# Optimization experiments

Measured on AMD Instinct MI355X. Metric: run time of the kernel, lower is better.

Reference implementation:

```python
import jax, jax.numpy as jnp
import numpy as np

B, N, T = 64, 256, 512          # batch, num_objs, num_triples
DO, DP, H, DOUT = 512, 512, 512, 512


def setup_inputs() -> dict:
    key = jax.random.key(0)
    ks = jax.random.split(key, 12)

    def kaiming(k, shape):
        fan_in = shape[0]
        return jax.random.normal(k, shape, jnp.float32) * np.sqrt(2.0 / fan_in)

    return {
        "obj_vecs": jax.random.normal(ks[0], (B, N, DO), jnp.float32),
        "pred_vecs": jax.random.normal(ks[1], (B, T, DP), jnp.float32),
        "edges": jax.random.randint(ks[2], (B, T, 3), 0, N, jnp.int64),
        # net1: [2*DO+DP -> H -> 2*H+DOUT], ReLU after each Linear
        "n1_w1": kaiming(ks[3], (2 * DO + DP, H)),
        "n1_b1": jnp.zeros((H,), jnp.float32),
        "n1_w2": kaiming(ks[4], (H, 2 * H + DOUT)),
        "n1_b2": jnp.zeros((2 * H + DOUT,), jnp.float32),
        # net2: [H -> H -> DOUT], ReLU after each Linear
        "n2_w1": kaiming(ks[5], (H, H)),
        "n2_b1": jnp.zeros((H,), jnp.float32),
        "n2_w2": kaiming(ks[6], (H, DOUT)),
        "n2_b2": jnp.zeros((DOUT,), jnp.float32),
    }


def reference(obj_vecs, pred_vecs, edges,
              n1_w1, n1_b1, n1_w2, n1_b2,
              n2_w1, n2_b1, n2_w2, n2_b2):
    num_batch, num_objs, _ = obj_vecs.shape
    h_dim = n1_b1.shape[0]
    d_out = n2_w2.shape[1]

    s_idx = edges[:, :, 0]            # [B, T] subject node ids
    o_idx = edges[:, :, 2]            # [B, T] object node ids

    # gather subject/object vectors per triple
    cur_s = jnp.take_along_axis(obj_vecs, s_idx[:, :, None], axis=1)  # [B,T,DO]
    cur_o = jnp.take_along_axis(obj_vecs, o_idx[:, :, None], axis=1)  # [B,T,DO]
    cur_t = jnp.concatenate([cur_s, pred_vecs, cur_o], axis=-1)       # [B,T,2DO+DP]

    # net1 MLP (Linear+ReLU, Linear+ReLU)
    hid = jax.nn.relu(jnp.einsum('btd,dh->bth', cur_t, n1_w1) + n1_b1)
    new_t = jax.nn.relu(jnp.einsum('bth,hk->btk', hid, n1_w2) + n1_b2)

    new_s = new_t[:, :, :h_dim]
    new_p = new_t[:, :, h_dim:h_dim + d_out]
    new_o = new_t[:, :, h_dim + d_out:2 * h_dim + d_out]

    # scatter-add back to nodes, per batch element
    b_ix = jnp.arange(num_batch)[:, None]            # [B,1]
    pooled = jnp.zeros((num_batch, num_objs, h_dim), obj_vecs.dtype)
    pooled = pooled.at[b_ix, s_idx].add(new_s)
    pooled = pooled.at[b_ix, o_idx].add(new_o)

    # avg pooling: divide by per-node incidence count (clamped at 1)
    ones = jnp.ones(s_idx.shape, obj_vecs.dtype)
    counts = jnp.zeros((num_batch, num_objs), obj_vecs.dtype)
    counts = counts.at[b_ix, s_idx].add(ones)
    counts = counts.at[b_ix, o_idx].add(ones)
    counts = jnp.maximum(counts, 1.0)
    pooled = pooled / counts[:, :, None]

    # net2 MLP (Linear+ReLU, Linear+ReLU)
    h2 = jax.nn.relu(jnp.einsum('bnh,hk->bnk', pooled, n2_w1) + n2_b1)
    new_obj_vecs = jax.nn.relu(jnp.einsum('bnh,hd->bnd', h2, n2_w2) + n2_b2)

    return new_obj_vecs, new_p
```

## Files before the change

### kernel.cpp

```cpp
#include <hip/hip_runtime.h>

typedef __bf16 bf16;
typedef __attribute__((ext_vector_type(4))) __bf16 bf16x4;
typedef __attribute__((ext_vector_type(8))) __bf16 bf16x8;
typedef __attribute__((ext_vector_type(4))) float f32x4;

#define DEVINL __device__ __forceinline__

typedef __attribute__((address_space(1))) void gvoid_t;
typedef __attribute__((address_space(3))) void lvoid_t;

DEVINL void async_ld16(const void* g, void* l) {
    __builtin_amdgcn_global_load_lds((gvoid_t*)g, (lvoid_t*)l, 16, 0, 0);
}

template<int MODE, int NBN>
__global__ __launch_bounds__(256, 2) void gemm_k(
    const bf16* __restrict__ A, const bf16* __restrict__ Bt,
    const float* __restrict__ bias, bf16* __restrict__ Dbf,
    float* __restrict__ Df, bf16* __restrict__ Dbf2,
    const int* __restrict__ edges, const bf16* __restrict__ obj,
    const bf16* __restrict__ pred, int K)
{
    const int tid = threadIdx.x;
    const int id = blockIdx.x;
    const int bn = (id >> 3) % NBN;
    const int bm = (id & 7) + 8 * ((id >> 3) / NBN);

    __shared__ __align__(16) bf16 ldsA[128 * 64];
    __shared__ __align__(16) bf16 ldsB[128 * 64];

    const int g_slot = tid & 7;
    const int row0 = tid >> 3;

    unsigned offS[4], offP[4], offO[4], offA[4], offB[4];
#pragma unroll
    for (int i = 0; i < 4; i++) {
        int r = row0 + 32 * i;
        int gr = bm * 128 + r;
        if (MODE == 0) {
            int b = gr >> 9;
            int s = edges[gr * 3 + 0] & 255;
            int o = edges[gr * 3 + 2] & 255;
            offS[i] = (unsigned)(b * 256 + s) * 512u;
            offP[i] = (unsigned)gr * 512u;
            offO[i] = (unsigned)(b * 256 + o) * 512u;
        } else {
            offA[i] = (unsigned)gr * (unsigned)K;
        }
        offB[i] = (unsigned)(bn * 128 + r) * (unsigned)K;
    }

    f32x4 acc[4][4];
    const f32x4 zero4 = {0.f, 0.f, 0.f, 0.f};
#pragma unroll
    for (int i = 0; i < 4; i++)
#pragma unroll
        for (int j = 0; j < 4; j++) acc[i][j] = zero4;

    const int wave = tid >> 6;
    const int lane = tid & 63;
    const int wr = (wave >> 1) * 64;
    const int wc = (wave & 1) * 64;
    const int lq = lane >> 4;
    const int lr = lane & 15;

    const int KT = K >> 6;
    for (int kt = 0; kt < KT; ++kt) {
        __syncthreads();
#pragma unroll
        for (int i = 0; i < 4; i++) {
            int r = row0 + 32 * i;
            int gsrc = g_slot ^ (r & 7);
            const bf16* gp;
            if (MODE == 0) {
                int region = kt >> 3;
                unsigned col = (unsigned)((kt & 7) * 64 + gsrc * 8);
                if (region == 0)      gp = obj + offS[i] + col;
                else if (region == 1) gp = pred + offP[i] + col;
                else                  gp = obj + offO[i] + col;
            } else {
                gp = A + offA[i] + (unsigned)(kt * 64 + gsrc * 8);
            }
            async_ld16(gp, ldsA + (tid + i * 256) * 8);
        }
#pragma unroll
        for (int i = 0; i < 4; i++) {
            int r = row0 + 32 * i;
            int gsrc = g_slot ^ (r & 7);
            async_ld16(Bt + offB[i] + (unsigned)(kt * 64 + gsrc * 8),
                       ldsB + (tid + i * 256) * 8);
        }
        __syncthreads();

#pragma unroll
        for (int ks = 0; ks < 2; ++ks) {
            bf16x8 af[4], bfr[4];
#pragma unroll
            for (int mi = 0; mi < 4; ++mi) {
                int r = wr + mi * 16 + lr;
                int g = (ks * 4 + lq) ^ (r & 7);
                af[mi] = *(const bf16x8*)(ldsA + (r * 8 + g) * 8);
            }
#pragma unroll
            for (int ni = 0; ni < 4; ++ni) {
                int r = wc + ni * 16 + lr;
                int g = (ks * 4 + lq) ^ (r & 7);
                bfr[ni] = *(const bf16x8*)(ldsB + (r * 8 + g) * 8);
            }
#pragma unroll
            for (int mi = 0; mi < 4; ++mi)
#pragma unroll
                for (int ni = 0; ni < 4; ++ni)
                    acc[mi][ni] = __builtin_amdgcn_mfma_f32_16x16x32_bf16(
                        bfr[ni], af[mi], acc[mi][ni], 0, 0, 0);
        }
    }

#pragma unroll
    for (int ni = 0; ni < 4; ++ni) {
        int col = bn * 128 + wc + ni * 16 + lq * 4;
        const f32x4 bv = *(const f32x4*)(bias + col);
#pragma unroll
        for (int mi = 0; mi < 4; ++mi) {
            int row = bm * 128 + wr + mi * 16 + lr;
            f32x4 v = acc[mi][ni];
            f32x4 x;
#pragma unroll
            for (int r = 0; r < 4; r++) {
                float t = v[r] + bv[r];
                x[r] = t > 0.f ? t : 0.f;
            }
            if (MODE == 1) {
                if (col < 512) {
                    bf16x4 o = { (bf16)x[0], (bf16)x[1], (bf16)x[2], (bf16)x[3] };
                    *(bf16x4*)(Dbf + row * 512 + col) = o;
                } else if (col < 1024) {
                    *(f32x4*)(Df + row * 512 + (col - 512)) = x;
                } else {
                    bf16x4 o = { (bf16)x[0], (bf16)x[1], (bf16)x[2], (bf16)x[3] };
                    *(bf16x4*)(Dbf2 + row * 512 + (col - 1024)) = o;
                }
            } else if (MODE == 3) {
                *(f32x4*)(Df + row * 512 + col) = x;
            } else {
                bf16x4 o = { (bf16)x[0], (bf16)x[1], (bf16)x[2], (bf16)x[3] };
                *(bf16x4*)(Dbf + row * 512 + col) = o;
            }
        }
    }
}

__global__ void cvt2_k(const float4* __restrict__ o, const float4* __restrict__ p,
                       bf16x4* __restrict__ ob, bf16x4* __restrict__ pb) {
    int i = blockIdx.x * 256 + threadIdx.x;
    if (i < 2097152) {
        float4 v = o[i];
        bf16x4 r = { (bf16)v.x, (bf16)v.y, (bf16)v.z, (bf16)v.w };
        ob[i] = r;
    } else {
        int j = i - 2097152;
        float4 v = p[j];
        bf16x4 r = { (bf16)v.x, (bf16)v.y, (bf16)v.z, (bf16)v.w };
        pb[j] = r;
    }
}

__global__ void transpose4_k(const float* __restrict__ w1, bf16* __restrict__ w1t,
                             const float* __restrict__ w2, bf16* __restrict__ w2t,
                             const float* __restrict__ w3, bf16* __restrict__ w3t,
                             const float* __restrict__ w4, bf16* __restrict__ w4t) {
    __shared__ float tile[32][33];
    int id = blockIdx.x;
    const float* src; bf16* dst; int R, C, bx, by;
    if (id < 768)       { src = w1; dst = w1t; R = 1536; C = 512;  bx = id % 16; by = id / 16; }
    else if (id < 1536) { id -= 768;  src = w2; dst = w2t; R = 512; C = 1536; bx = id % 48; by = id / 48; }
    else if (id < 1792) { id -= 1536; src = w3; dst = w3t; R = 512; C = 512;  bx = id % 16; by = id / 16; }
    else                { id -= 1792; src = w4; dst = w4t; R = 512; C = 512;  bx = id % 16; by = id / 16; }
    int c0 = bx * 32, r0 = by * 32;
    int tx = threadIdx.x, ty = threadIdx.y;
#pragma unroll
    for (int i = 0; i < 4; i++)
        tile[ty + i * 8][tx] = src[(size_t)(r0 + ty + i * 8) * C + c0 + tx];
    __syncthreads();
#pragma unroll
    for (int i = 0; i < 4; i++)
        dst[(size_t)(c0 + ty + i * 8) * R + r0 + tx] = (bf16)tile[tx][ty + i * 8];
}

__global__ void csr_k(const int* __restrict__ edges, int* __restrict__ counts_g,
                      int* __restrict__ starts_g, int* __restrict__ entries) {
    __shared__ int cnt[256];
    __shared__ int s[256];
    __shared__ int cur[256];
    int b = blockIdx.x, t = threadIdx.x;
    cnt[t] = 0;
    __syncthreads();
#pragma unroll
    for (int e = 0; e < 2; e++) {
        int row = b * 512 + t + e * 256;
        atomicAdd(&cnt[edges[row * 3 + 0] & 255], 1);
        atomicAdd(&cnt[edges[row * 3 + 2] & 255], 1);
    }
    __syncthreads();
    int c0 = cnt[t];
    s[t] = c0;
    __syncthreads();
#pragma unroll
    for (int off = 1; off < 256; off <<= 1) {
        int v = (t >= off) ? s[t - off] : 0;
        __syncthreads();
        s[t] += v;
        __syncthreads();
    }
    int excl = s[t] - c0;
    counts_g[b * 256 + t] = c0;
    starts_g[b * 256 + t] = b * 1024 + excl;
    cur[t] = excl;
    __syncthreads();
#pragma unroll
    for (int e = 0; e < 2; e++) {
        int row = b * 512 + t + e * 256;
        int si = edges[row * 3 + 0] & 255;
        int oi = edges[row * 3 + 2] & 255;
        int ps = atomicAdd(&cur[si], 1);
        entries[b * 1024 + ps] = row << 1;
        int po = atomicAdd(&cur[oi], 1);
        entries[b * 1024 + po] = (row << 1) | 1;
    }
}

__global__ void pool_k(const int* __restrict__ entries, const int* __restrict__ starts,
                       const int* __restrict__ counts,
                       const bf16* __restrict__ new_s, const bf16* __restrict__ new_o,
                       bf16* __restrict__ out) {
    __shared__ int ent[1024];
    int idx = blockIdx.x;
    int t = threadIdx.x;
    int c = counts[idx], st = starts[idx];
    for (int j = t; j < c; j += 256) ent[j] = entries[st + j];
    __syncthreads();
    float a0 = 0.f, a1 = 0.f;
    for (int j = 0; j < c; ++j) {
        int v = ent[j];
        const bf16* rp = ((v & 1) ? new_o : new_s) + (unsigned)(v >> 1) * 512u;
        a0 += (float)rp[t];
        a1 += (float)rp[t + 256];
    }
    float inv = 1.f / (float)(c > 1 ? c : 1);
    out[(unsigned)idx * 512u + t]       = (bf16)(a0 * inv);
    out[(unsigned)idx * 512u + t + 256] = (bf16)(a1 * inv);
}

extern "C" void kernel_launch(void* const* d_in, const int* in_sizes, int n_in,
                              void* d_out, int out_size, void* d_ws, size_t ws_size,
                              hipStream_t stream) {
    const float* obj_f  = (const float*)d_in[0];
    const float* pred_f = (const float*)d_in[1];
    const int*   edges  = (const int*)d_in[2];
    const float* w1 = (const float*)d_in[3];
    const float* b1 = (const float*)d_in[4];
    const float* w2 = (const float*)d_in[5];
    const float* b2 = (const float*)d_in[6];
    const float* w3 = (const float*)d_in[7];
    const float* b3 = (const float*)d_in[8];
    const float* w4 = (const float*)d_in[9];
    const float* b4 = (const float*)d_in[10];

    char* ws = (char*)d_ws;
    bf16* obj_bf  = (bf16*)(ws + 0);
    bf16* pred_bf = (bf16*)(ws + 16777216);
    bf16* new_s   = (bf16*)(ws + 0);
    int* entries  = (int*)(ws + 33554432);
    int* counts   = (int*)(ws + 33816576);
    int* starts   = (int*)(ws + 33882112);
    bf16* w1t = (bf16*)(ws + 50331648);
    bf16* w2t = (bf16*)(ws + 51904512);
    bf16* w3t = (bf16*)(ws + 53477376);
    bf16* w4t = (bf16*)(ws + 54001664);
    bf16* hid = (bf16*)(ws + 54525952);
    bf16* pooled_bf = hid;
    bf16* h2  = (bf16*)(ws + 71303168);

    float* out_obj = (float*)d_out;
    float* out_p   = (float*)d_out + 8388608;
    bf16* new_o    = (bf16*)d_out;

    cvt2_k<<<24576, 256, 0, stream>>>((const float4*)obj_f, (const float4*)pred_f,
                                      (bf16x4*)obj_bf, (bf16x4*)pred_bf);
    transpose4_k<<<2048, dim3(32, 8), 0, stream>>>(w1, w1t, w2, w2t, w3, w3t, w4, w4t);

    gemm_k<0, 4><<<1024, 256, 0, stream>>>(
        nullptr, w1t, b1, hid, nullptr, nullptr, edges, obj_bf, pred_bf, 1536);

    csr_k<<<64, 256, 0, stream>>>(edges, counts, starts, entries);

    gemm_k<1, 12><<<3072, 256, 0, stream>>>(
        hid, w2t, b2, new_s, out_p, new_o, nullptr, nullptr, nullptr, 512);

    pool_k<<<16384, 256, 0, stream>>>(entries, starts, counts, new_s, new_o, pooled_bf);

    gemm_k<2, 4><<<512, 256, 0, stream>>>(
        pooled_bf, w3t, b3, h2, nullptr, nullptr, nullptr, nullptr, nullptr, 512);
    gemm_k<3, 4><<<512, 256, 0, stream>>>(
        h2, w4t, b4, nullptr, out_obj, nullptr, nullptr, nullptr, nullptr, 512);
}
```

Before: 392.2 us.

## Fuse scatter-mean pooling into GEMM epilogue via float atomics

Replaces the CSR build and gather-based pooling kernels with fp32 atomic adds issued directly from the net1 second-layer GEMM epilogue into a zeroed pooled buffer. Node incidence counts are computed in extra blocks of the conversion kernel. The net2 first GEMM loads fp32 pooled rows, applies the 1/count scaling and converts to bf16 while staging into LDS. This removes two kernels and the bf16 intermediate round trip, at the cost of a large memset, many global atomics, nondeterministic summation order and a synchronous A load path.

```diff
diff --git a/kernel.cpp b/kernel.cpp
--- a/kernel.cpp
+++ b/kernel.cpp
@@ -14,13 +14,19 @@
     __builtin_amdgcn_global_load_lds((gvoid_t*)g, (lvoid_t*)l, 16, 0, 0);
 }
 
+DEVINL void atomic_add_f32_dev(float* p, float v) {
+    asm volatile("global_atomic_add_f32 %0, %1, off sc1"
+                 :: "v"(p), "v"(v) : "memory");
+}
+
 template<int MODE, int NBN>
 __global__ __launch_bounds__(256, 2) void gemm_k(
     const bf16* __restrict__ A, const bf16* __restrict__ Bt,
     const float* __restrict__ bias, bf16* __restrict__ Dbf,
-    float* __restrict__ Df, bf16* __restrict__ Dbf2,
+    float* __restrict__ Df, float* __restrict__ Dpool,
     const int* __restrict__ edges, const bf16* __restrict__ obj,
-    const bf16* __restrict__ pred, int K)
+    const bf16* __restrict__ pred, const float* __restrict__ Af,
+    const int* __restrict__ counts, int K)
 {
     const int tid = threadIdx.x;
     const int id = blockIdx.x;
@@ -34,6 +40,7 @@
     const int row0 = tid >> 3;
 
     unsigned offS[4], offP[4], offO[4], offA[4], offB[4];
+    float invc4[4];
 #pragma unroll
     for (int i = 0; i < 4; i++) {
         int r = row0 + 32 * i;
@@ -47,6 +54,10 @@
             offO[i] = (unsigned)(b * 256 + o) * 512u;
         } else {
             offA[i] = (unsigned)gr * (unsigned)K;
+            if (MODE == 4) {
+                int c = counts[gr];
+                invc4[i] = 1.f / (float)(c > 1 ? c : 1);
+            }
         }
         offB[i] = (unsigned)(bn * 128 + r) * (unsigned)K;
     }
@@ -72,17 +83,30 @@
         for (int i = 0; i < 4; i++) {
             int r = row0 + 32 * i;
             int gsrc = g_slot ^ (r & 7);
-            const bf16* gp;
-            if (MODE == 0) {
-                int region = kt >> 3;
-                unsigned col = (unsigned)((kt & 7) * 64 + gsrc * 8);
-                if (region == 0)      gp = obj + offS[i] + col;
-                else if (region == 1) gp = pred + offP[i] + col;
-                else                  gp = obj + offO[i] + col;
+            if (MODE == 4) {
+                const float* gp = Af + offA[i] + (unsigned)(kt * 64 + gsrc * 8);
+                float4 v0 = *(const float4*)gp;
+                float4 v1 = *(const float4*)(gp + 4);
+                float sc = invc4[i];
+                bf16x8 w;
+                w[0] = (bf16)(v0.x * sc); w[1] = (bf16)(v0.y * sc);
+                w[2] = (bf16)(v0.z * sc); w[3] = (bf16)(v0.w * sc);
+                w[4] = (bf16)(v1.x * sc); w[5] = (bf16)(v1.y * sc);
+                w[6] = (bf16)(v1.z * sc); w[7] = (bf16)(v1.w * sc);
+                *(bf16x8*)(ldsA + (tid + i * 256) * 8) = w;
             } else {
-                gp = A + offA[i] + (unsigned)(kt * 64 + gsrc * 8);
-            }
-            async_ld16(gp, ldsA + (tid + i * 256) * 8);
+                const bf16* gp;
+                if (MODE == 0) {
+                    int region = kt >> 3;
+                    unsigned col = (unsigned)((kt & 7) * 64 + gsrc * 8);
+                    if (region == 0)      gp = obj + offS[i] + col;
+                    else if (region == 1) gp = pred + offP[i] + col;
+                    else                  gp = obj + offO[i] + col;
+                } else {
+                    gp = A + offA[i] + (unsigned)(kt * 64 + gsrc * 8);
+                }
+                async_ld16(gp, ldsA + (tid + i * 256) * 8);
+            }
         }
 #pragma unroll
         for (int i = 0; i < 4; i++) {
@@ -117,6 +141,18 @@
         }
     }
 
+    unsigned sB[4], oB[4];
+    if (MODE == 1) {
+#pragma unroll
+        for (int mi = 0; mi < 4; ++mi) {
+            int row = bm * 128 + wr + mi * 16 + lr;
+            int b = row >> 9;
+            int s = edges[row * 3 + 0] & 255;
+            int o = edges[row * 3 + 2] & 255;
+            sB[mi] = (unsigned)((b << 8) + s) * 512u;
+            oB[mi] = (unsigned)((b << 8) + o) * 512u;
+        }
+    }
 #pragma unroll
     for (int ni = 0; ni < 4; ++ni) {
         int col = bn * 128 + wc + ni * 16 + lq * 4;
@@ -133,13 +169,19 @@
             }
             if (MODE == 1) {
                 if (col < 512) {
-                    bf16x4 o = { (bf16)x[0], (bf16)x[1], (bf16)x[2], (bf16)x[3] };
-                    *(bf16x4*)(Dbf + row * 512 + col) = o;
+                    float* p = Dpool + sB[mi] + col;
+                    atomic_add_f32_dev(p + 0, x[0]);
+                    atomic_add_f32_dev(p + 1, x[1]);
+                    atomic_add_f32_dev(p + 2, x[2]);
+                    atomic_add_f32_dev(p + 3, x[3]);
                 } else if (col < 1024) {
                     *(f32x4*)(Df + row * 512 + (col - 512)) = x;
                 } else {
-                    bf16x4 o = { (bf16)x[0], (bf16)x[1], (bf16)x[2], (bf16)x[3] };
-                    *(bf16x4*)(Dbf2 + row * 512 + (col - 1024)) = o;
+                    float* p = Dpool + oB[mi] + (col - 1024);
+                    atomic_add_f32_dev(p + 0, x[0]);
+                    atomic_add_f32_dev(p + 1, x[1]);
+                    atomic_add_f32_dev(p + 2, x[2]);
+                    atomic_add_f32_dev(p + 3, x[3]);
                 }
             } else if (MODE == 3) {
                 *(f32x4*)(Df + row * 512 + col) = x;
@@ -152,8 +194,26 @@
 }
 
 __global__ void cvt2_k(const float4* __restrict__ o, const float4* __restrict__ p,
-                       bf16x4* __restrict__ ob, bf16x4* __restrict__ pb) {
-    int i = blockIdx.x * 256 + threadIdx.x;
+                       bf16x4* __restrict__ ob, bf16x4* __restrict__ pb,
+                       const int* __restrict__ edges, int* __restrict__ counts_g) {
+    int blk = blockIdx.x;
+    int t = threadIdx.x;
+    if (blk >= 24576) {
+        __shared__ int cnt[256];
+        int b = blk - 24576;
+        cnt[t] = 0;
+        __syncthreads();
+#pragma unroll
+        for (int e = 0; e < 2; e++) {
+            int row = b * 512 + t + e * 256;
+            atomicAdd(&cnt[edges[row * 3 + 0] & 255], 1);
+            atomicAdd(&cnt[edges[row * 3 + 2] & 255], 1);
+        }
+        __syncthreads();
+        counts_g[b * 256 + t] = cnt[t];
+        return;
+    }
+    int i = blk * 256 + t;
     if (i < 2097152) {
         float4 v = o[i];
         bf16x4 r = { (bf16)v.x, (bf16)v.y, (bf16)v.z, (bf16)v.w };
@@ -186,70 +246,6 @@
 #pragma unroll
     for (int i = 0; i < 4; i++)
         dst[(size_t)(c0 + ty + i * 8) * R + r0 + tx] = (bf16)tile[tx][ty + i * 8];
-}
-
-__global__ void csr_k(const int* __restrict__ edges, int* __restrict__ counts_g,
-                      int* __restrict__ starts_g, int* __restrict__ entries) {
-    __shared__ int cnt[256];
-    __shared__ int s[256];
-    __shared__ int cur[256];
-    int b = blockIdx.x, t = threadIdx.x;
-    cnt[t] = 0;
-    __syncthreads();
-#pragma unroll
-    for (int e = 0; e < 2; e++) {
-        int row = b * 512 + t + e * 256;
-        atomicAdd(&cnt[edges[row * 3 + 0] & 255], 1);
-        atomicAdd(&cnt[edges[row * 3 + 2] & 255], 1);
-    }
-    __syncthreads();
-    int c0 = cnt[t];
-    s[t] = c0;
-    __syncthreads();
-#pragma unroll
-    for (int off = 1; off < 256; off <<= 1) {
-        int v = (t >= off) ? s[t - off] : 0;
-        __syncthreads();
-        s[t] += v;
-        __syncthreads();
-    }
-    int excl = s[t] - c0;
-    counts_g[b * 256 + t] = c0;
-    starts_g[b * 256 + t] = b * 1024 + excl;
-    cur[t] = excl;
-    __syncthreads();
-#pragma unroll
-    for (int e = 0; e < 2; e++) {
-        int row = b * 512 + t + e * 256;
-        int si = edges[row * 3 + 0] & 255;
-        int oi = edges[row * 3 + 2] & 255;
-        int ps = atomicAdd(&cur[si], 1);
-        entries[b * 1024 + ps] = row << 1;
-        int po = atomicAdd(&cur[oi], 1);
-        entries[b * 1024 + po] = (row << 1) | 1;
-    }
-}
-
-__global__ void pool_k(const int* __restrict__ entries, const int* __restrict__ starts,
-                       const int* __restrict__ counts,
-                       const bf16* __restrict__ new_s, const bf16* __restrict__ new_o,
-                       bf16* __restrict__ out) {
-    __shared__ int ent[1024];
-    int idx = blockIdx.x;
-    int t = threadIdx.x;
-    int c = counts[idx], st = starts[idx];
-    for (int j = t; j < c; j += 256) ent[j] = entries[st + j];
-    __syncthreads();
-    float a0 = 0.f, a1 = 0.f;
-    for (int j = 0; j < c; ++j) {
-        int v = ent[j];
-        const bf16* rp = ((v & 1) ? new_o : new_s) + (unsigned)(v >> 1) * 512u;
-        a0 += (float)rp[t];
-        a1 += (float)rp[t + 256];
-    }
-    float inv = 1.f / (float)(c > 1 ? c : 1);
-    out[(unsigned)idx * 512u + t]       = (bf16)(a0 * inv);
-    out[(unsigned)idx * 512u + t + 256] = (bf16)(a1 * inv);
 }
 
 extern "C" void kernel_launch(void* const* d_in, const int* in_sizes, int n_in,
@@ -270,38 +266,38 @@
     char* ws = (char*)d_ws;
     bf16* obj_bf  = (bf16*)(ws + 0);
     bf16* pred_bf = (bf16*)(ws + 16777216);
-    bf16* new_s   = (bf16*)(ws + 0);
-    int* entries  = (int*)(ws + 33554432);
-    int* counts   = (int*)(ws + 33816576);
-    int* starts   = (int*)(ws + 33882112);
+    float* pooled = (float*)(ws + 0);
     bf16* w1t = (bf16*)(ws + 50331648);
     bf16* w2t = (bf16*)(ws + 51904512);
     bf16* w3t = (bf16*)(ws + 53477376);
     bf16* w4t = (bf16*)(ws + 54001664);
     bf16* hid = (bf16*)(ws + 54525952);
-    bf16* pooled_bf = hid;
     bf16* h2  = (bf16*)(ws + 71303168);
 
     float* out_obj = (float*)d_out;
     float* out_p   = (float*)d_out + 8388608;
-    bf16* new_o    = (bf16*)d_out;
-
-    cvt2_k<<<24576, 256, 0, stream>>>((const float4*)obj_f, (const float4*)pred_f,
-                                      (bf16x4*)obj_bf, (bf16x4*)pred_bf);
+    int* counts    = (int*)d_out;
+
+    cvt2_k<<<24640, 256, 0, stream>>>((const float4*)obj_f, (const float4*)pred_f,
+                                      (bf16x4*)obj_bf, (bf16x4*)pred_bf,
+                                      edges, counts);
     transpose4_k<<<2048, dim3(32, 8), 0, stream>>>(w1, w1t, w2, w2t, w3, w3t, w4, w4t);
 
     gemm_k<0, 4><<<1024, 256, 0, stream>>>(
-        nullptr, w1t, b1, hid, nullptr, nullptr, edges, obj_bf, pred_bf, 1536);
-
-    csr_k<<<64, 256, 0, stream>>>(edges, counts, starts, entries);
+        nullptr, w1t, b1, hid, nullptr, nullptr, edges, obj_bf, pred_bf,
+        nullptr, nullptr, 1536);
+
+    hipMemsetAsync(pooled, 0, 33554432, stream);
 
     gemm_k<1, 12><<<3072, 256, 0, stream>>>(
-        hid, w2t, b2, new_s, out_p, new_o, nullptr, nullptr, nullptr, 512);
-
-    pool_k<<<16384, 256, 0, stream>>>(entries, starts, counts, new_s, new_o, pooled_bf);
-
-    gemm_k<2, 4><<<512, 256, 0, stream>>>(
-        pooled_bf, w3t, b3, h2, nullptr, nullptr, nullptr, nullptr, nullptr, 512);
+        hid, w2t, b2, nullptr, out_p, pooled, edges, nullptr, nullptr,
+        nullptr, nullptr, 512);
+
+    gemm_k<4, 4><<<512, 256, 0, stream>>>(
+        nullptr, w3t, b3, h2, nullptr, nullptr, nullptr, nullptr, nullptr,
+        pooled, counts, 512);
+
     gemm_k<3, 4><<<512, 256, 0, stream>>>(
-        h2, w4t, b4, nullptr, out_obj, nullptr, nullptr, nullptr, nullptr, 512);
-}
+        h2, w4t, b4, nullptr, out_obj, nullptr, nullptr, nullptr, nullptr,
+        nullptr, nullptr, 512);
+}
```

Measured after the change: 756.9 us. 93.0% more time.

## Replace CSR build and gather pooling with LDS atomic scatter pooling; merge prep kernels

Applied to the files above, without the earlier changes.

Drops the separate CSR-building kernel and the per-node gather pool kernel. In their place, a single pool kernel has each block own one batch element and a 64-column slice. It scatter-adds new_s and new_o rows into a float accumulator in shared memory with LDS atomics, then divides by per-node counts. The bf16 input conversion and the weight-transpose kernels are also merged into one launch to cut launch overhead. In exchange, summation order becomes nondeterministic. Shared-memory use is large (about 70KB per block), and only 512 blocks run, each issuing narrow 128-byte reads per wave.

```diff
diff --git a/kernel.cpp b/kernel.cpp
--- a/kernel.cpp
+++ b/kernel.cpp
@@ -151,9 +151,34 @@
     }
 }
 
-__global__ void cvt2_k(const float4* __restrict__ o, const float4* __restrict__ p,
-                       bf16x4* __restrict__ ob, bf16x4* __restrict__ pb) {
-    int i = blockIdx.x * 256 + threadIdx.x;
+__global__ void pre_k(const float4* __restrict__ o, const float4* __restrict__ p,
+                      bf16x4* __restrict__ ob, bf16x4* __restrict__ pb,
+                      const float* __restrict__ w1, bf16* __restrict__ w1t,
+                      const float* __restrict__ w2, bf16* __restrict__ w2t,
+                      const float* __restrict__ w3, bf16* __restrict__ w3t,
+                      const float* __restrict__ w4, bf16* __restrict__ w4t) {
+    __shared__ float tile[32][33];
+    int blk = blockIdx.x;
+    int t = threadIdx.x;
+    if (blk >= 24576) {
+        int id = blk - 24576;
+        const float* src; bf16* dst; int R, C, bx, by;
+        if (id < 768)       { src = w1; dst = w1t; R = 1536; C = 512;  bx = id % 16; by = id / 16; }
+        else if (id < 1536) { id -= 768;  src = w2; dst = w2t; R = 512; C = 1536; bx = id % 48; by = id / 48; }
+        else if (id < 1792) { id -= 1536; src = w3; dst = w3t; R = 512; C = 512;  bx = id % 16; by = id / 16; }
+        else                { id -= 1792; src = w4; dst = w4t; R = 512; C = 512;  bx = id % 16; by = id / 16; }
+        int c0 = bx * 32, r0 = by * 32;
+        int tx = t & 31, ty = t >> 5;
+#pragma unroll
+        for (int i = 0; i < 4; i++)
+            tile[ty + i * 8][tx] = src[(size_t)(r0 + ty + i * 8) * C + c0 + tx];
+        __syncthreads();
+#pragma unroll
+        for (int i = 0; i < 4; i++)
+            dst[(size_t)(c0 + ty + i * 8) * R + r0 + tx] = (bf16)tile[tx][ty + i * 8];
+        return;
+    }
+    int i = blk * 256 + t;
     if (i < 2097152) {
         float4 v = o[i];
         bf16x4 r = { (bf16)v.x, (bf16)v.y, (bf16)v.z, (bf16)v.w };
@@ -166,90 +191,55 @@
     }
 }
 
-__global__ void transpose4_k(const float* __restrict__ w1, bf16* __restrict__ w1t,
-                             const float* __restrict__ w2, bf16* __restrict__ w2t,
-                             const float* __restrict__ w3, bf16* __restrict__ w3t,
-                             const float* __restrict__ w4, bf16* __restrict__ w4t) {
-    __shared__ float tile[32][33];
-    int id = blockIdx.x;
-    const float* src; bf16* dst; int R, C, bx, by;
-    if (id < 768)       { src = w1; dst = w1t; R = 1536; C = 512;  bx = id % 16; by = id / 16; }
-    else if (id < 1536) { id -= 768;  src = w2; dst = w2t; R = 512; C = 1536; bx = id % 48; by = id / 48; }
-    else if (id < 1792) { id -= 1536; src = w3; dst = w3t; R = 512; C = 512;  bx = id % 16; by = id / 16; }
-    else                { id -= 1792; src = w4; dst = w4t; R = 512; C = 512;  bx = id % 16; by = id / 16; }
-    int c0 = bx * 32, r0 = by * 32;
-    int tx = threadIdx.x, ty = threadIdx.y;
-#pragma unroll
-    for (int i = 0; i < 4; i++)
-        tile[ty + i * 8][tx] = src[(size_t)(r0 + ty + i * 8) * C + c0 + tx];
-    __syncthreads();
-#pragma unroll
-    for (int i = 0; i < 4; i++)
-        dst[(size_t)(c0 + ty + i * 8) * R + r0 + tx] = (bf16)tile[tx][ty + i * 8];
-}
-
-__global__ void csr_k(const int* __restrict__ edges, int* __restrict__ counts_g,
-                      int* __restrict__ starts_g, int* __restrict__ entries) {
+__global__ __launch_bounds__(256, 2) void pool2_k(
+    const int* __restrict__ edges,
+    const bf16* __restrict__ new_s, const bf16* __restrict__ new_o,
+    bf16* __restrict__ out) {
+    __shared__ float acc[256 * 64];
+    __shared__ int sidx[512], oidx[512];
     __shared__ int cnt[256];
-    __shared__ int s[256];
-    __shared__ int cur[256];
-    int b = blockIdx.x, t = threadIdx.x;
+    const int b = blockIdx.x >> 3;
+    const int ch = blockIdx.x & 7;
+    const int t = threadIdx.x;
+
+#pragma unroll
+    for (int i = 0; i < 64; i++) acc[t + i * 256] = 0.f;
     cnt[t] = 0;
     __syncthreads();
-#pragma unroll
-    for (int e = 0; e < 2; e++) {
-        int row = b * 512 + t + e * 256;
-        atomicAdd(&cnt[edges[row * 3 + 0] & 255], 1);
-        atomicAdd(&cnt[edges[row * 3 + 2] & 255], 1);
+
+#pragma unroll
+    for (int e0 = 0; e0 < 2; e0++) {
+        int e = t + e0 * 256;
+        int row = b * 512 + e;
+        int s = edges[row * 3 + 0] & 255;
+        int o = edges[row * 3 + 2] & 255;
+        sidx[e] = s;
+        oidx[e] = o;
+        atomicAdd(&cnt[s], 1);
+        atomicAdd(&cnt[o], 1);
     }
     __syncthreads();
-    int c0 = cnt[t];
-    s[t] = c0;
+
+    const int wv = t >> 6, ln = t & 63;
+    const unsigned c = (unsigned)(ch * 64 + ln);
+    for (int e = wv; e < 512; e += 4) {
+        unsigned row = (unsigned)(b * 512 + e);
+        float vs = (float)new_s[row * 512u + c];
+        atomicAdd(&acc[sidx[e] * 64 + ln], vs);
+        float vo = (float)new_o[row * 512u + c];
+        atomicAdd(&acc[oidx[e] * 64 + ln], vo);
+    }
     __syncthreads();
-#pragma unroll
-    for (int off = 1; off < 256; off <<= 1) {
-        int v = (t >= off) ? s[t - off] : 0;
-        __syncthreads();
-        s[t] += v;
-        __syncthreads();
-    }
-    int excl = s[t] - c0;
-    counts_g[b * 256 + t] = c0;
-    starts_g[b * 256 + t] = b * 1024 + excl;
-    cur[t] = excl;
-    __syncthreads();
-#pragma unroll
-    for (int e = 0; e < 2; e++) {
-        int row = b * 512 + t + e * 256;
-        int si = edges[row * 3 + 0] & 255;
-        int oi = edges[row * 3 + 2] & 255;
-        int ps = atomicAdd(&cur[si], 1);
-        entries[b * 1024 + ps] = row << 1;
-        int po = atomicAdd(&cur[oi], 1);
-        entries[b * 1024 + po] = (row << 1) | 1;
-    }
-}
-
-__global__ void pool_k(const int* __restrict__ entries, const int* __restrict__ starts,
-                       const int* __restrict__ counts,
-                       const bf16* __restrict__ new_s, const bf16* __restrict__ new_o,
-                       bf16* __restrict__ out) {
-    __shared__ int ent[1024];
-    int idx = blockIdx.x;
-    int t = threadIdx.x;
-    int c = counts[idx], st = starts[idx];
-    for (int j = t; j < c; j += 256) ent[j] = entries[st + j];
-    __syncthreads();
-    float a0 = 0.f, a1 = 0.f;
-    for (int j = 0; j < c; ++j) {
-        int v = ent[j];
-        const bf16* rp = ((v & 1) ? new_o : new_s) + (unsigned)(v >> 1) * 512u;
-        a0 += (float)rp[t];
-        a1 += (float)rp[t + 256];
-    }
-    float inv = 1.f / (float)(c > 1 ? c : 1);
-    out[(unsigned)idx * 512u + t]       = (bf16)(a0 * inv);
-    out[(unsigned)idx * 512u + t + 256] = (bf16)(a1 * inv);
+
+#pragma unroll
+    for (int i = 0; i < 64; i++) {
+        int idx = i * 256 + t;
+        int n = idx >> 6, col = idx & 63;
+        int cn = cnt[n];
+        float inv = 1.f / (float)(cn > 1 ? cn : 1);
+        out[(unsigned)(b * 256 + n) * 512u + (unsigned)(ch * 64 + col)] =
+            (bf16)(acc[idx] * inv);
+    }
 }
 
 extern "C" void kernel_launch(void* const* d_in, const int* in_sizes, int n_in,
@@ -271,9 +261,6 @@
     bf16* obj_bf  = (bf16*)(ws + 0);
     bf16* pred_bf = (bf16*)(ws + 16777216);
     bf16* new_s   = (bf16*)(ws + 0);
-    int* entries  = (int*)(ws + 33554432);
-    int* counts   = (int*)(ws + 33816576);
-    int* starts   = (int*)(ws + 33882112);
     bf16* w1t = (bf16*)(ws + 50331648);
     bf16* w2t = (bf16*)(ws + 51904512);
     bf16* w3t = (bf16*)(ws + 53477376);
@@ -286,22 +273,21 @@
     float* out_p   = (float*)d_out + 8388608;
     bf16* new_o    = (bf16*)d_out;
 
-    cvt2_k<<<24576, 256, 0, stream>>>((const float4*)obj_f, (const float4*)pred_f,
-                                      (bf16x4*)obj_bf, (bf16x4*)pred_bf);
-    transpose4_k<<<2048, dim3(32, 8), 0, stream>>>(w1, w1t, w2, w2t, w3, w3t, w4, w4t);
+    pre_k<<<26624, 256, 0, stream>>>((const float4*)obj_f, (const float4*)pred_f,
+                                     (bf16x4*)obj_bf, (bf16x4*)pred_bf,
+                                     w1, w1t, w2, w2t, w3, w3t, w4, w4t);
 
     gemm_k<0, 4><<<1024, 256, 0, stream>>>(
         nullptr, w1t, b1, hid, nullptr, nullptr, edges, obj_bf, pred_bf, 1536);
 
-    csr_k<<<64, 256, 0, stream>>>(edges, counts, starts, entries);
-
     gemm_k<1, 12><<<3072, 256, 0, stream>>>(
         hid, w2t, b2, new_s, out_p, new_o, nullptr, nullptr, nullptr, 512);
 
-    pool_k<<<16384, 256, 0, stream>>>(entries, starts, counts, new_s, new_o, pooled_bf);
+    pool2_k<<<512, 256, 0, stream>>>(edges, new_s, new_o, pooled_bf);
 
     gemm_k<2, 4><<<512, 256, 0, stream>>>(
         pooled_bf, w3t, b3, h2, nullptr, nullptr, nullptr, nullptr, nullptr, 512);
+
     gemm_k<3, 4><<<512, 256, 0, stream>>>(
         h2, w4t, b4, nullptr, out_obj, nullptr, nullptr, nullptr, nullptr, 512);
 }
```

Result: slower. 535.7 us (+36.6%).
